# Kernel tuning notes

Measured on AMD Instinct MI355X. Metric: run time of the kernel, lower is better.

The kernel has to match this reference:

```python
import jax, jax.numpy as jnp
import numpy as np

EPS = 1e-5

def layer_norm(x, gamma, beta):
    m = x.mean(axis=-1, keepdims=True)
    v = ((x - m) ** 2).mean(axis=-1, keepdims=True)  # correction=0
    return (x - m) / jnp.sqrt(v + EPS) * gamma + beta

def setup_inputs() -> dict:
    key = jax.random.key(0)
    B, T, E, H = 2, 2048, 1024, 16
    hd = E // H
    dff = 4 * E
    ks = jax.random.split(key, 10)
    s = 0.02
    return {
        "x": jax.random.normal(ks[0], (B, T, E), jnp.float32),
        "wq": jax.random.normal(ks[1], (H, E, hd), jnp.float32) * s,
        "wk": jax.random.normal(ks[2], (H, E, hd), jnp.float32) * s,
        "wv": jax.random.normal(ks[3], (H, E, hd), jnp.float32) * s,
        "w_proj": jax.random.normal(ks[4], (E, E), jnp.float32) * s,
        "b_proj": jnp.zeros((E,), jnp.float32),
        "gamma1": jnp.ones((E,), jnp.float32),
        "beta1": jnp.zeros((E,), jnp.float32),
        "gamma2": jnp.ones((E,), jnp.float32),
        "beta2": jnp.zeros((E,), jnp.float32),
        "w1": jax.random.normal(ks[5], (E, dff), jnp.float32) * s,
        "b1": jnp.zeros((dff,), jnp.float32),
        "w2": jax.random.normal(ks[6], (dff, E), jnp.float32) * s,
        "b2": jnp.zeros((E,), jnp.float32),
    }

def reference(x, wq, wk, wv, w_proj, b_proj, gamma1, beta1, gamma2, beta2, w1, b1, w2, b2):
    B, T, E = x.shape
    H, _, hd = wq.shape
    # pre-attention norm; NOTE: residual uses the normalized value (as in source)
    h = layer_norm(x, gamma1, beta1)
    # per-head projections, vectorized over heads: [B,H,T,hd]
    q = jnp.einsum('bte,hek->bhtk', h, wq)
    k = jnp.einsum('bte,hek->bhtk', h, wk)
    v = jnp.einsum('bte,hek->bhtk', h, wv)
    att = jnp.einsum('bhtk,bhsk->bhts', q, k) / jnp.sqrt(jnp.float32(hd))
    causal = jnp.tril(jnp.ones((T, T), bool))
    att = jnp.where(causal, att, -jnp.inf)
    p = jax.nn.softmax(att, axis=-1)  # dropout is identity in eval
    o = jnp.einsum('bhts,bhsk->bhtk', p, v)
    o = o.transpose(0, 2, 1, 3).reshape(B, T, E)  # concat heads
    attn_out = o @ w_proj + b_proj
    x2 = h + attn_out
    # pre-FFN norm; residual again uses normalized value
    h2 = layer_norm(x2, gamma2, beta2)
    ffn = jax.nn.relu(h2 @ w1 + b1) @ w2 + b2
    return h2 + ffn
```

## Files before the change

kernel.cpp:

```cpp
#include <hip/hip_runtime.h>
#include <stdint.h>

typedef unsigned short u16;
typedef __attribute__((ext_vector_type(8))) short short8;
typedef __attribute__((ext_vector_type(4))) short short4_t;
typedef __attribute__((ext_vector_type(4))) float f32x4;

__device__ __forceinline__ float b2f(u16 u){ union{unsigned i; float f;}v; v.i=((unsigned)u)<<16; return v.f; }
__device__ __forceinline__ u16 f2b(float f){ unsigned x=__float_as_uint(f); return (u16)((x + 0x7fffu + ((x>>16)&1u))>>16); }

#if __has_builtin(__builtin_amdgcn_exp2f)
#define EXP2F(x) __builtin_amdgcn_exp2f(x)
#else
#define EXP2F(x) exp2f(x)
#endif

#if __has_builtin(__builtin_amdgcn_mfma_f32_16x16x16_bf16)
#define MFMA16(a,b,c) __builtin_amdgcn_mfma_f32_16x16x16_bf16(a,b,c,0,0,0)
#elif __has_builtin(__builtin_amdgcn_mfma_f32_16x16x16bf16_1k)
#define MFMA16(a,b,c) __builtin_amdgcn_mfma_f32_16x16x16bf16_1k(a,b,c,0,0,0)
#else
static __device__ __forceinline__ f32x4 mfma16_asm(short4_t a, short4_t b, f32x4 c){
  __asm__("v_mfma_f32_16x16x16_bf16 %0, %1, %2, %3" : "=v"(c) : "v"(a), "v"(b), "0"(c));
  return c;
}
#define MFMA16(a,b,c) mfma16_asm(a,b,c)
#endif

__device__ __forceinline__ void async16(const void* g, void* l){
  __builtin_amdgcn_global_load_lds((const __attribute__((address_space(1))) void*)g,
                                   (__attribute__((address_space(3))) void*)l, 16, 0, 0);
}

__device__ __forceinline__ short4_t pack4(f32x4 s){
  unsigned u0 = (__float_as_uint(s[0]) + 0x8000u) >> 16;
  unsigned u1 = (__float_as_uint(s[1]) + 0x8000u) & 0xffff0000u;
  unsigned u2 = (__float_as_uint(s[2]) + 0x8000u) >> 16;
  unsigned u3 = (__float_as_uint(s[3]) + 0x8000u) & 0xffff0000u;
  union { unsigned v[2]; short4_t s4; } r;
  r.v[0] = u0 | u1; r.v[1] = u2 | u3;
  return r.s4;
}

template<int IN_F32>
__global__ __launch_bounds__(256) void ln_kernel(const void* __restrict__ xin,
    const float* __restrict__ g, const float* __restrict__ b, u16* __restrict__ y)
{
  const int E = 1024;
  int row = blockIdx.x, t = threadIdx.x;
  float f0,f1,f2,f3;
  if (IN_F32){
    const float* xr = (const float*)xin + (size_t)row*E;
    float4 xv = *(const float4*)(xr + t*4);
    f0=xv.x; f1=xv.y; f2=xv.z; f3=xv.w;
  } else {
    const u16* xr = (const u16*)xin + (size_t)row*E;
    ushort4 xv = *(const ushort4*)(xr + t*4);
    f0=b2f(xv.x); f1=b2f(xv.y); f2=b2f(xv.z); f3=b2f(xv.w);
  }
  float s1 = f0+f1+f2+f3;
  float s2 = f0*f0+f1*f1+f2*f2+f3*f3;
  #pragma unroll
  for (int off=32; off>=1; off>>=1){ s1 += __shfl_xor(s1,off); s2 += __shfl_xor(s2,off); }
  __shared__ float red[8];
  int w = t>>6;
  if ((t&63)==0){ red[w]=s1; red[4+w]=s2; }
  __syncthreads();
  float S1 = red[0]+red[1]+red[2]+red[3];
  float S2 = red[4]+red[5]+red[6]+red[7];
  float mean = S1*(1.0f/E);
  float var  = S2*(1.0f/E) - mean*mean;
  float inv  = rsqrtf(var + 1e-5f);
  float4 gv = *(const float4*)(g + t*4);
  float4 bv = *(const float4*)(b + t*4);
  ushort4 o;
  o.x = f2b((f0-mean)*inv*gv.x+bv.x);
  o.y = f2b((f1-mean)*inv*gv.y+bv.y);
  o.z = f2b((f2-mean)*inv*gv.z+bv.z);
  o.w = f2b((f3-mean)*inv*gv.w+bv.w);
  *(ushort4*)(y + (size_t)row*E + t*4) = o;
}

__global__ __launch_bounds__(256) void transpose_bt(const float* __restrict__ src, u16* __restrict__ dst,
                                                    int ld_src, int ld_dst)
{
  __shared__ u16 tile[64*66];
  int c0 = blockIdx.x*64, r0 = blockIdx.y*64;
  int t = threadIdx.x;
  #pragma unroll
  for (int i=0;i<16;++i){
    int lin = i*256 + t;
    int rr = lin>>6, cc = lin&63;
    tile[cc*66+rr] = f2b(src[(size_t)(r0+rr)*ld_src + c0+cc]);
  }
  __syncthreads();
  #pragma unroll
  for (int i=0;i<16;++i){
    int lin = i*256 + t;
    int cc = lin>>6, rr = lin&63;
    dst[(size_t)(c0+cc)*ld_dst + r0+rr] = tile[cc*66+rr];
  }
}

__global__ __launch_bounds__(256) void qkv_repack(const float* __restrict__ wq, const float* __restrict__ wk,
                                                  const float* __restrict__ wv, u16* __restrict__ dst)
{
  __shared__ u16 tile[64*66];
  int e0 = blockIdx.x*64;
  int sel = blockIdx.y>>4, h = blockIdx.y&15;
  const float* src = (sel==0?wq:(sel==1?wk:wv)) + (size_t)h*1024*64;
  int t = threadIdx.x;
  #pragma unroll
  for (int i=0;i<16;++i){
    int lin=i*256+t; int rr=lin>>6, cc=lin&63;
    tile[cc*66+rr] = f2b(src[(size_t)(e0+rr)*64 + cc]);
  }
  __syncthreads();
  #pragma unroll
  for (int i=0;i<16;++i){
    int lin=i*256+t; int cc=lin>>6, rr=lin&63;
    dst[(size_t)(sel*1024 + h*64 + cc)*1024 + e0+rr] = tile[cc*66+rr];
  }
}

__global__ __launch_bounds__(256) void vtrans(const u16* __restrict__ qkv, u16* __restrict__ VT)
{
  __shared__ u16 tile[64*66];
  int bh = blockIdx.y, bb = bh>>4, h = bh&15;
  int s0 = blockIdx.x*64;
  const u16* src = qkv + ((size_t)(bb*2048) + s0)*3072 + 2048 + h*64;
  int t = threadIdx.x;
  int sr = t>>3, c0 = (t&7)*8;
  #pragma unroll
  for (int half=0; half<2; ++half){
    const u16* p = src + (size_t)(sr+half*32)*3072 + c0;
    ushort4 v0 = *(const ushort4*)p;
    ushort4 v1 = *(const ushort4*)(p+4);
    uint* d = (uint*)(tile + (sr+half*32)*66 + c0);
    d[0] = (uint)v0.x | ((uint)v0.y<<16);
    d[1] = (uint)v0.z | ((uint)v0.w<<16);
    d[2] = (uint)v1.x | ((uint)v1.y<<16);
    d[3] = (uint)v1.z | ((uint)v1.w<<16);
  }
  __syncthreads();
  u16* out = VT + (size_t)bh*64*2048 + s0;
  int dw = t>>3, sc = (t&7)*8;
  #pragma unroll
  for (int half=0; half<2; ++half){
    int d = dw + half*32;
    short8 pk;
    #pragma unroll
    for (int j=0;j<8;++j) pk[j] = (short)tile[(sc+j)*66 + d];
    *(short8*)(out + (size_t)d*2048 + sc) = pk;
  }
}

template<int MI>
__global__ __launch_bounds__(256, 3) void gemm_bt(const u16* __restrict__ A, const u16* __restrict__ Bt,
    u16* __restrict__ C, float* __restrict__ Cf, int M, int N, int K,
    const float* __restrict__ bias, const u16* __restrict__ residual, int do_relu, int gx)
{
  __shared__ __align__(16) u16 As[2][MI*32*64];
  __shared__ __align__(16) u16 Bs[2][128*64];
  int t = threadIdx.x;
  int bid = blockIdx.y * gridDim.x + blockIdx.x;
  int xcd = bid & 7, slot = bid >> 3;
  int gy = 8 / gx;
  int rx = gridDim.x / gx, ry = gridDim.y / gy;
  int col_b = (xcd % gx) * rx + (slot % rx);
  int row_b = (xcd / gx) * ry + (slot / rx);
  int row0 = row_b*(MI*32), col0 = col_b*128;
  int l = t&63, w = t>>6;
  int wm = (w>>1)*(MI*16), wn = (w&1)*64;
  int lr = l&15, lq = l>>4;
  (void)M;

  f32x4 acc[MI][4];
  #pragma unroll
  for (int i=0;i<MI;++i)
    #pragma unroll
    for (int j=0;j<4;++j) acc[i][j] = f32x4{0.f,0.f,0.f,0.f};

  const u16* gA = A  + (size_t)(row0 + (t>>3))*K + (((t&7)^((t>>3)&7))<<3);
  const u16* gB = Bt + (size_t)(col0 + (t>>3))*K + (((t&7)^((t>>3)&7))<<3);
  const size_t rnd = (size_t)32*K;
  int nk = K>>6;

  #pragma unroll
  for (int r=0;r<MI;++r) async16(gA + r*rnd, As[0] + r*2048 + t*8);
  #pragma unroll
  for (int r=0;r<4;++r)  async16(gB + r*rnd, Bs[0] + r*2048 + t*8);

  int sw8 = (lr&7);
  for (int kt=0; kt<nk; ++kt){
    int cur = kt&1;
    __syncthreads();
    if (kt+1 < nk){
      int ko = (kt+1)<<6;
      #pragma unroll
      for (int r=0;r<MI;++r) async16(gA + r*rnd + ko, As[cur^1] + r*2048 + t*8);
      #pragma unroll
      for (int r=0;r<4;++r)  async16(gB + r*rnd + ko, Bs[cur^1] + r*2048 + t*8);
    }
    const u16* as = As[cur];
    const u16* bs = Bs[cur];
    #pragma unroll
    for (int kk=0;kk<2;++kk){
      int so = (((kk*4+lq)^sw8))<<3;
      short8 a[MI], b[4];
      #pragma unroll
      for (int i=0;i<MI;++i) a[i] = *(const short8*)(as + (wm+i*16+lr)*64 + so);
      #pragma unroll
      for (int j=0;j<4;++j)  b[j] = *(const short8*)(bs + (wn+j*16+lr)*64 + so);
      #pragma unroll
      for (int i=0;i<MI;++i)
        #pragma unroll
        for (int j=0;j<4;++j)
          acc[i][j] = __builtin_amdgcn_mfma_f32_16x16x32_bf16(a[i], b[j], acc[i][j], 0,0,0);
    }
  }

  #pragma unroll
  for (int i=0;i<MI;++i){
    #pragma unroll
    for (int j=0;j<4;++j){
      int col = col0 + wn + j*16 + lr;
      float bv = bias ? bias[col] : 0.0f;
      #pragma unroll
      for (int r=0;r<4;++r){
        int row = row0 + wm + i*16 + lq*4 + r;
        float v = acc[i][j][r] + bv;
        if (do_relu) v = fmaxf(v, 0.0f);
        if (residual) v += b2f(residual[(size_t)row*N + col]);
        if (Cf) Cf[(size_t)row*N + col] = v;
        else    C [(size_t)row*N + col] = f2b(v);
      }
    }
  }
}

__global__ __launch_bounds__(512,2) void gemm256(const u16* __restrict__ A, const u16* __restrict__ Bt,
    u16* __restrict__ C, float* __restrict__ Cf, int N, int K,
    const float* __restrict__ bias, const u16* __restrict__ residual, int do_relu, int gx)
{
  __shared__ __align__(16) u16 As[2][256*64];
  __shared__ __align__(16) u16 Bs[2][256*64];
  int t = threadIdx.x;
  int bid = blockIdx.y*gridDim.x + blockIdx.x;
  int xcd = bid & 7, slot = bid >> 3;
  int gy = 8/gx;
  int rx = gridDim.x/gx, ry = gridDim.y/gy;
  int col_b = (xcd%gx)*rx + slot%rx;
  int row_b = (xcd/gx)*ry + slot/rx;
  int row0 = row_b*256, col0 = col_b*256;
  int l = t&63, w = t>>6;
  int wr = w>>2, wc = w&3;
  int lr = l&15, lq = l>>4, sw = lr&7;

  f32x4 acc[8][4];
  #pragma unroll
  for (int m=0;m<8;++m)
    #pragma unroll
    for (int n=0;n<4;++n) acc[m][n] = f32x4{0.f,0.f,0.f,0.f};

  int i = t>>3, c8 = t&7;
  int swc = (c8 ^ (i&7))*8;
  const u16* aS[4]; const u16* bS[4];
  {
    int la[4] = { i, 128+i, 64+i, 192+i };
    #pragma unroll
    for (int s=0;s<4;++s){
      aS[s] = A + (size_t)(row0 + la[s])*K + swc;
      int p = s*64 + i;
      int lb = ((p>>5)&3)*64 + (p>>7)*32 + (p&31);
      bS[s] = Bt + (size_t)(col0 + lb)*K + swc;
    }
  }
  int nk = K>>6;

  async16(aS[0], As[0] + 0*4096 + t*8);
  async16(aS[1], As[0] + 1*4096 + t*8);
  async16(bS[0], Bs[0] + 0*4096 + t*8);
  async16(bS[1], Bs[0] + 1*4096 + t*8);
  async16(bS[2], Bs[0] + 2*4096 + t*8);
  async16(bS[3], Bs[0] + 3*4096 + t*8);
  async16(aS[2], As[0] + 2*4096 + t*8);
  async16(aS[3], As[0] + 3*4096 + t*8);
  asm volatile("s_waitcnt vmcnt(4)" ::: "memory");
  __builtin_amdgcn_s_barrier();

  short8 af[4][2], bf[2][2];

#define RD_A(qm) \
  _Pragma("unroll") \
  for (int mm=0;mm<4;++mm){ \
    _Pragma("unroll") \
    for (int kk=0;kk<2;++kk) \
      af[mm][kk] = *(const short8*)(asC + ((qm)*128 + wr*64 + mm*16 + lr)*64 + (((kk*4+lq)^sw)<<3)); \
  }
#define RD_B(qn) \
  _Pragma("unroll") \
  for (int nn=0;nn<2;++nn){ \
    _Pragma("unroll") \
    for (int kk=0;kk<2;++kk) \
      bf[nn][kk] = *(const short8*)(bsC + ((qn)*128 + wc*32 + nn*16 + lr)*64 + (((kk*4+lq)^sw)<<3)); \
  }
#define MMQ(qm,qn) \
  __builtin_amdgcn_s_setprio(1); \
  _Pragma("unroll") \
  for (int mm=0;mm<4;++mm){ \
    _Pragma("unroll") \
    for (int nn=0;nn<2;++nn){ \
      _Pragma("unroll") \
      for (int kk=0;kk<2;++kk) \
        acc[(qm)*4+mm][(qn)*2+nn] = __builtin_amdgcn_mfma_f32_16x16x32_bf16(af[mm][kk], bf[nn][kk], acc[(qm)*4+mm][(qn)*2+nn], 0,0,0); \
    } \
  } \
  __builtin_amdgcn_s_setprio(0);
#define BARW \
  __builtin_amdgcn_s_barrier(); \
  asm volatile("s_waitcnt lgkmcnt(0)" ::: "memory"); \
  __builtin_amdgcn_sched_barrier(0);
#define PIN __builtin_amdgcn_sched_barrier(0);

  for (int kt=0; kt<nk-1; ++kt){
    int cur = kt&1;
    const u16* asC = As[cur]; const u16* bsC = Bs[cur];
    u16* asN = As[cur^1];    u16* bsN = Bs[cur^1];
    int ko = (kt+1)<<6;
    RD_A(0); RD_B(0);
    async16(aS[0]+ko, asN + 0*4096 + t*8);
    async16(aS[1]+ko, asN + 1*4096 + t*8);
    async16(bS[0]+ko, bsN + 0*4096 + t*8);
    async16(bS[1]+ko, bsN + 1*4096 + t*8);
    async16(bS[2]+ko, bsN + 2*4096 + t*8);
    async16(bS[3]+ko, bsN + 3*4096 + t*8);
    async16(aS[2]+ko, asN + 2*4096 + t*8);
    async16(aS[3]+ko, asN + 3*4096 + t*8);
    PIN;
    asm volatile("s_waitcnt vmcnt(10)" ::: "memory");
    BARW;
    MMQ(0,0);
    __builtin_amdgcn_s_barrier();
    RD_B(1);
    PIN;
    asm volatile("s_waitcnt vmcnt(8)" ::: "memory");
    BARW;
    MMQ(0,1);
    __builtin_amdgcn_s_barrier();
    RD_A(1);
    PIN;
    BARW;
    MMQ(1,1);
    __builtin_amdgcn_s_barrier();
    RD_B(0);
    PIN;
    asm volatile("s_waitcnt vmcnt(4)" ::: "memory");
    BARW;
    MMQ(1,0);
    __builtin_amdgcn_s_barrier();
  }
  {
    int cur = (nk-1)&1;
    const u16* asC = As[cur]; const u16* bsC = Bs[cur];
    RD_A(0); RD_B(0);
    asm volatile("s_waitcnt vmcnt(2)" ::: "memory");
    BARW;
    MMQ(0,0);
    __builtin_amdgcn_s_barrier();
    RD_B(1);
    asm volatile("s_waitcnt vmcnt(0)" ::: "memory");
    BARW;
    MMQ(0,1);
    __builtin_amdgcn_s_barrier();
    RD_A(1);
    BARW;
    MMQ(1,1);
    __builtin_amdgcn_s_barrier();
    RD_B(0);
    BARW;
    MMQ(1,0);
  }
#undef RD_A
#undef RD_B
#undef MMQ
#undef BARW
#undef PIN

  #pragma unroll
  for (int m=0;m<8;++m){
    #pragma unroll
    for (int n=0;n<4;++n){
      int col = col0 + wc*64 + n*16 + lr;
      float bv = bias ? bias[col] : 0.0f;
      #pragma unroll
      for (int r=0;r<4;++r){
        int row = row0 + wr*128 + m*16 + lq*4 + r;
        float v = acc[m][n][r] + bv;
        if (do_relu) v = fmaxf(v, 0.0f);
        if (residual) v += b2f(residual[(size_t)row*N + col]);
        if (Cf) Cf[(size_t)row*N + col] = v;
        else    C [(size_t)row*N + col] = f2b(v);
      }
    }
  }
}

__global__ __launch_bounds__(256,4) void attn_kernel(const u16* __restrict__ QKV,
    const u16* __restrict__ VT, u16* __restrict__ O)
{
  const int T=2048, LD=3072, E=1024;
  int bid = blockIdx.y * gridDim.x + blockIdx.x;
  int xcd = bid & 7, slot = bid >> 3;
  int idx = slot & 31, grp = slot >> 5;
  int qt = (grp & 1) ? idx : 31 - idx;
  int bh = xcd*4 + grp;
  int bb = bh>>4, h = bh&15;
  const u16* base = QKV + (size_t)bb*T*LD;
  const u16* Qp = base + h*64;
  const u16* Kp = base + 1024 + h*64;
  const u16* Vtp = VT + (size_t)bh*64*2048;
  int t = threadIdx.x, l = t&63, w = t>>6;
  int lr = l&15, lq = l>>4;

  __shared__ __align__(16) u16 Ks[2][64*64];
  __shared__ __align__(16) u16 Vs[2][64*64];

  const float QSC = 0.125f*1.44269504f;
  int q0 = qt*64 + w*16;
  short8 aq[2];
  #pragma unroll
  for (int kk=0;kk<2;++kk){
    short8 raw = *(const short8*)(Qp + (size_t)(q0+lr)*LD + kk*32 + lq*8);
    short8 sc;
    #pragma unroll
    for (int j=0;j<8;++j) sc[j] = (short)f2b(b2f((u16)raw[j])*QSC);
    aq[kk]=sc;
  }

  float mrun = -3e38f, lrun = 0.f;
  f32x4 Oacc[4];
  #pragma unroll
  for (int dt=0;dt<4;++dt) Oacc[dt] = f32x4{0.f,0.f,0.f,0.f};

  int kc = (l&7) ^ (l>>3);
  int ra = 8*w + (l>>3);

  async16(Kp  + (size_t)ra*LD        + kc*8, Ks[0] + t*8);
  async16(Kp  + (size_t)(ra+32)*LD   + kc*8, Ks[0] + 2048 + t*8);
  async16(Vtp + (size_t)ra*2048      + kc*8, Vs[0] + t*8);
  async16(Vtp + (size_t)(ra+32)*2048 + kc*8, Vs[0] + 2048 + t*8);

  for (int it=0; it<=qt; ++it){
    int s0 = it*64, cur = it&1;
    __syncthreads();
    if (it < qt){
      int sn = s0+64;
      u16* kd = Ks[cur^1]; u16* vd = Vs[cur^1];
      async16(Kp  + (size_t)(sn+ra)*LD        + kc*8, kd + t*8);
      async16(Kp  + (size_t)(sn+ra+32)*LD     + kc*8, kd + 2048 + t*8);
      async16(Vtp + (size_t)ra*2048      + sn + kc*8, vd + t*8);
      async16(Vtp + (size_t)(ra+32)*2048 + sn + kc*8, vd + 2048 + t*8);
    }
    const u16* ks = Ks[cur];
    const u16* vs = Vs[cur];

    f32x4 S[4];
    #pragma unroll
    for (int st=0; st<4; ++st){
      short8 kf0 = *(const short8*)(ks + (st*16+lr)*64 + ((lq  )^(lr&7))*8);
      short8 kf1 = *(const short8*)(ks + (st*16+lr)*64 + ((4+lq)^(lr&7))*8);
      f32x4 z = f32x4{0.f,0.f,0.f,0.f};
      z = __builtin_amdgcn_mfma_f32_16x16x32_bf16(kf0, aq[0], z, 0,0,0);
      z = __builtin_amdgcn_mfma_f32_16x16x32_bf16(kf1, aq[1], z, 0,0,0);
      S[st] = z;
    }
    if (it == qt){
      int qg = q0 + lr;
      #pragma unroll
      for (int st=0;st<4;++st)
        #pragma unroll
        for (int r=0;r<4;++r){
          int sg = s0 + st*16 + lq*4 + r;
          if (sg > qg) S[st][r] = -3e38f;
        }
    }
    float m = S[0][0];
    #pragma unroll
    for (int st=0;st<4;++st)
      #pragma unroll
      for (int r=0;r<4;++r) m = fmaxf(m, S[st][r]);
    m = fmaxf(m, __shfl_xor(m,16));
    m = fmaxf(m, __shfl_xor(m,32));
    float mnew = fmaxf(mrun, m);
    float alpha = EXP2F(mrun - mnew);
    mrun = mnew;
    float ssum = 0.f;
    #pragma unroll
    for (int st=0;st<4;++st)
      #pragma unroll
      for (int r=0;r<4;++r){ float p = EXP2F(S[st][r]-mnew); S[st][r]=p; ssum+=p; }
    ssum += __shfl_xor(ssum,16);
    ssum += __shfl_xor(ssum,32);
    lrun = lrun*alpha + ssum;
    short4_t pk[4];
    #pragma unroll
    for (int st=0;st<4;++st) pk[st] = pack4(S[st]);
    float af[4];
    #pragma unroll
    for (int r=0;r<4;++r) af[r] = __shfl(alpha, lq*4+r);
    #pragma unroll
    for (int dt=0;dt<4;++dt)
      #pragma unroll
      for (int r=0;r<4;++r) Oacc[dt][r] *= af[r];
    #pragma unroll
    for (int st=0;st<4;++st){
      #pragma unroll
      for (int dt=0;dt<4;++dt){
        short4_t vf = *(const short4_t*)(vs + (dt*16+lr)*64 + ((2*st+(lq>>1))^(lr&7))*8 + (lq&1)*4);
        Oacc[dt] = MFMA16(pk[st], vf, Oacc[dt]);
      }
    }
  }
  float linv[4];
  #pragma unroll
  for (int r=0;r<4;++r) linv[r] = 1.0f/__shfl(lrun, lq*4+r);
  #pragma unroll
  for (int dt=0;dt<4;++dt)
    #pragma unroll
    for (int r=0;r<4;++r){
      int qg = q0 + lq*4 + r;
      O[(size_t)(bb*T+qg)*E + h*64 + dt*16 + lr] = f2b(Oacc[dt][r]*linv[r]);
    }
}

extern "C" void kernel_launch(void* const* d_in, const int* in_sizes, int n_in,
                              void* d_out, int out_size, void* d_ws, size_t ws_size,
                              hipStream_t stream)
{
  (void)in_sizes; (void)n_in; (void)out_size; (void)ws_size;
  const float* x     = (const float*)d_in[0];
  const float* wq    = (const float*)d_in[1];
  const float* wk    = (const float*)d_in[2];
  const float* wv    = (const float*)d_in[3];
  const float* wproj = (const float*)d_in[4];
  const float* bproj = (const float*)d_in[5];
  const float* g1    = (const float*)d_in[6];
  const float* be1   = (const float*)d_in[7];
  const float* g2    = (const float*)d_in[8];
  const float* be2   = (const float*)d_in[9];
  const float* w1    = (const float*)d_in[10];
  const float* b1    = (const float*)d_in[11];
  const float* w2    = (const float*)d_in[12];
  const float* b2    = (const float*)d_in[13];
  float* out = (float*)d_out;

  char* ws = (char*)d_ws;
  size_t off = 0;
  auto alloc = [&](size_t bytes)->void*{ void* p = ws + off; off += (bytes + 255) & ~(size_t)255; return p; };
  u16* hnorm  = (u16*)alloc((size_t)4096*1024*2);
  u16* qkv    = (u16*)alloc((size_t)4096*3072*2);
  u16* VT     = (u16*)alloc((size_t)32*64*2048*2);
  u16* attnO  = (u16*)alloc((size_t)4096*1024*2);
  u16* x2     = (u16*)alloc((size_t)4096*1024*2);
  u16* h2     = (u16*)alloc((size_t)4096*1024*2);
  u16* ffn1   = (u16*)alloc((size_t)4096*4096*2);
  u16* wqkvT  = (u16*)alloc((size_t)3072*1024*2);
  u16* wprojT = (u16*)alloc((size_t)1024*1024*2);
  u16* w1T    = (u16*)alloc((size_t)4096*1024*2);
  u16* w2T    = (u16*)alloc((size_t)1024*4096*2);

  qkv_repack  <<<dim3(16,48),256,0,stream>>>(wq,wk,wv,wqkvT);
  transpose_bt<<<dim3(16,16),256,0,stream>>>(wproj, wprojT, 1024, 1024);
  transpose_bt<<<dim3(64,16),256,0,stream>>>(w1,    w1T,    4096, 1024);
  transpose_bt<<<dim3(16,64),256,0,stream>>>(w2,    w2T,    1024, 4096);

  ln_kernel<1><<<4096,256,0,stream>>>(x, g1, be1, hnorm);
  gemm256<<<dim3(12,16),512,0,stream>>>(hnorm, wqkvT, qkv, nullptr, 3072, 1024, nullptr, nullptr, 0, 4);
  vtrans<<<dim3(32,32),256,0,stream>>>(qkv, VT);
  attn_kernel<<<dim3(32,32),256,0,stream>>>(qkv, VT, attnO);
  gemm_bt<2><<<dim3(8,64),256,0,stream>>>(attnO, wprojT, x2, nullptr, 4096,1024,1024, bproj, hnorm, 0, 2);
  ln_kernel<0><<<4096,256,0,stream>>>(x2, g2, be2, h2);
  gemm256<<<dim3(16,16),512,0,stream>>>(h2, w1T, ffn1, nullptr, 4096, 1024, b1, nullptr, 1, 4);
  gemm_bt<2><<<dim3(8,64),256,0,stream>>>(ffn1, w2T, nullptr, out, 4096,1024,4096, b2, h2, 0, 2);
}
```

Baseline: 361.3 us.

## Deepen GEMM main-loop prefetch and double-buffer B fragments in registers

Restructures the 256x256 GEMM main loop so global-to-LDS loads are issued one to two K-tiles ahead, split into quarter-tile chunks interleaved with the MFMA quadrants. B fragments are now held in two register sets so the next tile's A/B reads overlap the last quadrant's MFMAs. The goal is to hide LDS and global latency better and drop some barrier stalls. The cost is more registers and tricky vmcnt/barrier ordering, which could cause races or lower occupancy.

```diff
diff --git a/kernel.cpp b/kernel.cpp
--- a/kernel.cpp
+++ b/kernel.cpp
@@ -278,34 +278,33 @@
   }
   int nk = K>>6;
 
-  async16(aS[0], As[0] + 0*4096 + t*8);
-  async16(aS[1], As[0] + 1*4096 + t*8);
-  async16(bS[0], Bs[0] + 0*4096 + t*8);
-  async16(bS[1], Bs[0] + 1*4096 + t*8);
-  async16(bS[2], Bs[0] + 2*4096 + t*8);
-  async16(bS[3], Bs[0] + 3*4096 + t*8);
-  async16(aS[2], As[0] + 2*4096 + t*8);
-  async16(aS[3], As[0] + 3*4096 + t*8);
-  asm volatile("s_waitcnt vmcnt(4)" ::: "memory");
-  __builtin_amdgcn_s_barrier();
-
-  short8 af[4][2], bf[2][2];
-
-#define RD_A(qm) \
+  u16* A0p = As[0]; u16* A1p = As[1];
+  u16* B0p = Bs[0]; u16* B1p = Bs[1];
+
+  short8 af[4][2], bP[2][2], bQ[2][2];
+
+#define VM8  asm volatile("s_waitcnt vmcnt(8)" ::: "memory");
+#define VM6  asm volatile("s_waitcnt vmcnt(6)" ::: "memory");
+#define VM0  asm volatile("s_waitcnt vmcnt(0)" ::: "memory");
+#define LGK  asm volatile("s_waitcnt lgkmcnt(0)" ::: "memory");
+#define BAR  __builtin_amdgcn_s_barrier();
+#define PIN  __builtin_amdgcn_sched_barrier(0);
+
+#define RD_A(BUF,qm) \
   _Pragma("unroll") \
   for (int mm=0;mm<4;++mm){ \
     _Pragma("unroll") \
     for (int kk=0;kk<2;++kk) \
-      af[mm][kk] = *(const short8*)(asC + ((qm)*128 + wr*64 + mm*16 + lr)*64 + (((kk*4+lq)^sw)<<3)); \
-  }
-#define RD_B(qn) \
+      af[mm][kk] = *(const short8*)((const u16*)(BUF) + ((qm)*128 + wr*64 + mm*16 + lr)*64 + (((kk*4+lq)^sw)<<3)); \
+  }
+#define RD_B(DST,BUF,qn) \
   _Pragma("unroll") \
   for (int nn=0;nn<2;++nn){ \
     _Pragma("unroll") \
     for (int kk=0;kk<2;++kk) \
-      bf[nn][kk] = *(const short8*)(bsC + ((qn)*128 + wc*32 + nn*16 + lr)*64 + (((kk*4+lq)^sw)<<3)); \
-  }
-#define MMQ(qm,qn) \
+      DST[nn][kk] = *(const short8*)((const u16*)(BUF) + ((qn)*128 + wc*32 + nn*16 + lr)*64 + (((kk*4+lq)^sw)<<3)); \
+  }
+#define MMQ(qm,qn,BSS) \
   __builtin_amdgcn_s_setprio(1); \
   _Pragma("unroll") \
   for (int mm=0;mm<4;++mm){ \
@@ -313,79 +312,84 @@
     for (int nn=0;nn<2;++nn){ \
       _Pragma("unroll") \
       for (int kk=0;kk<2;++kk) \
-        acc[(qm)*4+mm][(qn)*2+nn] = __builtin_amdgcn_mfma_f32_16x16x32_bf16(af[mm][kk], bf[nn][kk], acc[(qm)*4+mm][(qn)*2+nn], 0,0,0); \
+        acc[(qm)*4+mm][(qn)*2+nn] = __builtin_amdgcn_mfma_f32_16x16x32_bf16(af[mm][kk], BSS[nn][kk], acc[(qm)*4+mm][(qn)*2+nn], 0,0,0); \
     } \
   } \
   __builtin_amdgcn_s_setprio(0);
-#define BARW \
-  __builtin_amdgcn_s_barrier(); \
-  asm volatile("s_waitcnt lgkmcnt(0)" ::: "memory"); \
-  __builtin_amdgcn_sched_barrier(0);
-#define PIN __builtin_amdgcn_sched_barrier(0);
+
+  async16(aS[0], A0p + 0*4096 + t*8);
+  async16(aS[1], A0p + 1*4096 + t*8);
+  async16(bS[0], B0p + 0*4096 + t*8);
+  async16(bS[1], B0p + 1*4096 + t*8);
+  async16(bS[2], B0p + 2*4096 + t*8);
+  async16(bS[3], B0p + 3*4096 + t*8);
+  async16(aS[2], A0p + 2*4096 + t*8);
+  async16(aS[3], A0p + 3*4096 + t*8);
+  async16(aS[0]+64, A1p + 0*4096 + t*8);
+  async16(aS[1]+64, A1p + 1*4096 + t*8);
+  async16(bS[0]+64, B1p + 0*4096 + t*8);
+  async16(bS[1]+64, B1p + 1*4096 + t*8);
+  async16(bS[2]+64, B1p + 2*4096 + t*8);
+  async16(bS[3]+64, B1p + 3*4096 + t*8);
+  VM8; BAR;
+  RD_A(A0p, 0); RD_B(bP, B0p, 0); PIN;
 
   for (int kt=0; kt<nk-1; ++kt){
     int cur = kt&1;
-    const u16* asC = As[cur]; const u16* bsC = Bs[cur];
-    u16* asN = As[cur^1];    u16* bsN = Bs[cur^1];
-    int ko = (kt+1)<<6;
-    RD_A(0); RD_B(0);
-    async16(aS[0]+ko, asN + 0*4096 + t*8);
-    async16(aS[1]+ko, asN + 1*4096 + t*8);
-    async16(bS[0]+ko, bsN + 0*4096 + t*8);
-    async16(bS[1]+ko, bsN + 1*4096 + t*8);
-    async16(bS[2]+ko, bsN + 2*4096 + t*8);
-    async16(bS[3]+ko, bsN + 3*4096 + t*8);
-    async16(aS[2]+ko, asN + 2*4096 + t*8);
-    async16(aS[3]+ko, asN + 3*4096 + t*8);
-    PIN;
-    asm volatile("s_waitcnt vmcnt(10)" ::: "memory");
-    BARW;
-    MMQ(0,0);
-    __builtin_amdgcn_s_barrier();
-    RD_B(1);
-    PIN;
-    asm volatile("s_waitcnt vmcnt(8)" ::: "memory");
-    BARW;
-    MMQ(0,1);
-    __builtin_amdgcn_s_barrier();
-    RD_A(1);
-    PIN;
-    BARW;
-    MMQ(1,1);
-    __builtin_amdgcn_s_barrier();
-    RD_B(0);
-    PIN;
-    asm volatile("s_waitcnt vmcnt(4)" ::: "memory");
-    BARW;
-    MMQ(1,0);
-    __builtin_amdgcn_s_barrier();
+    u16* Ac = As[cur]; u16* Bc = Bs[cur];
+    u16* An = As[cur^1]; u16* Bn = Bs[cur^1];
+    int ko1 = (kt+1)<<6;
+    int kc2 = (kt+2 < nk) ? kt+2 : nk-1;
+    int ko2 = kc2<<6;
+    async16(aS[2]+ko1, An + 2*4096 + t*8);
+    async16(aS[3]+ko1, An + 3*4096 + t*8);
+    PIN; BAR; LGK; PIN;
+    MMQ(0,0,bP);
+    RD_B(bQ, Bc, 1); PIN;
+    BAR;
+    async16(bS[2]+ko2, Bc + 2*4096 + t*8);
+    async16(bS[3]+ko2, Bc + 3*4096 + t*8);
+    PIN; VM8; BAR; LGK; PIN;
+    MMQ(0,1,bQ);
+    RD_A(Ac, 1); PIN;
+    BAR;
+    async16(aS[0]+ko2, Ac + 0*4096 + t*8);
+    async16(aS[1]+ko2, Ac + 1*4096 + t*8);
+    PIN; BAR; LGK; PIN;
+    MMQ(1,1,bQ);
+    PIN; BAR;
+    async16(bS[0]+ko2, Bc + 0*4096 + t*8);
+    async16(bS[1]+ko2, Bc + 1*4096 + t*8);
+    PIN; VM8; BAR; LGK; PIN;
+    MMQ(1,0,bP);
+    RD_A(An, 0); RD_B(bP, Bn, 0); PIN;
+    BAR;
   }
   {
     int cur = (nk-1)&1;
-    const u16* asC = As[cur]; const u16* bsC = Bs[cur];
-    RD_A(0); RD_B(0);
-    asm volatile("s_waitcnt vmcnt(2)" ::: "memory");
-    BARW;
-    MMQ(0,0);
-    __builtin_amdgcn_s_barrier();
-    RD_B(1);
-    asm volatile("s_waitcnt vmcnt(0)" ::: "memory");
-    BARW;
-    MMQ(0,1);
-    __builtin_amdgcn_s_barrier();
-    RD_A(1);
-    BARW;
-    MMQ(1,1);
-    __builtin_amdgcn_s_barrier();
-    RD_B(0);
-    BARW;
-    MMQ(1,0);
-  }
+    u16* Ac = As[cur]; u16* Bc = Bs[cur];
+    BAR; LGK; PIN;
+    MMQ(0,0,bP);
+    RD_B(bQ, Bc, 1); PIN;
+    BAR;
+    VM6; BAR; LGK; PIN;
+    MMQ(0,1,bQ);
+    RD_A(Ac, 1); PIN;
+    LGK; PIN;
+    MMQ(1,1,bQ);
+    MMQ(1,0,bP);
+  }
+  VM0;
+
+#undef VM8
+#undef VM6
+#undef VM0
+#undef LGK
+#undef BAR
+#undef PIN
 #undef RD_A
 #undef RD_B
 #undef MMQ
-#undef BARW
-#undef PIN
 
   #pragma unroll
   for (int m=0;m<8;++m){
```

New measurement: 358.5 us. Within noise of the previous version (-0.8%).
